# Performance work log

Hardware: AMD Instinct MI355X
Metric: run time of the kernel (lower is better)

The kernel has to match this reference:

```python
import jax, jax.numpy as jnp
import numpy as np

NUM_KNOTS = 256
DEGREE = 3
NUM_BASIS = NUM_KNOTS - DEGREE - 1  # 252
N = 1_048_576


def setup_inputs() -> dict:
    key = jax.random.key(0)
    # evaluation points in [-pi, pi), shape [N, 1] like the torch module
    x = jax.random.uniform(key, (N, 1), jnp.float32, -np.pi, np.pi)
    # knot vector: constant buffer from __init__
    knots = jnp.linspace(-np.pi, np.pi, NUM_KNOTS, dtype=jnp.float32)
    return {"x": x, "knots": knots}


def reference(x, knots):
    """Cox-de Boor B-spline basis, computed bottom-up (dynamic programming).

    Mathematically identical to the naive recursion in the torch module:
    same indicator base case ([knots[j], knots[j+1])) and same denominator>0
    guards, but each level is computed once and fully vectorized over N and j.
    """
    xs = x[:, 0]  # [N]
    # degree-0 basis: indicator of half-open knot interval -> [N, K-1]
    B = ((knots[:-1] <= xs[:, None]) & (xs[:, None] < knots[1:])).astype(jnp.float32)
    for k in range(1, DEGREE + 1):
        m = NUM_KNOTS - 1 - k  # number of basis functions at level k
        d1 = knots[k:k + m] - knots[:m]          # knots[j+k]   - knots[j]
        d2 = knots[k + 1:k + 1 + m] - knots[1:1 + m]  # knots[j+k+1] - knots[j+1]
        w1 = jnp.where(d1 > 0, (xs[:, None] - knots[:m]) / jnp.where(d1 > 0, d1, 1.0), 0.0)
        w2 = jnp.where(d2 > 0, (knots[k + 1:k + 1 + m] - xs[:, None]) / jnp.where(d2 > 0, d2, 1.0), 0.0)
        B = w1 * B[:, :m] + w2 * B[:, 1:1 + m]
    # level DEGREE already has exactly NUM_BASIS columns
    return B[:, :NUM_BASIS]
```

## Files before the change

kernel.cpp:

```cpp
#include <hip/hip_runtime.h>


constexpr int NUM_KNOTS = 256;
constexpr int NUM_BASIS = 252;
constexpr int CHUNKS    = 63;
constexpr int ROWS      = 256;

typedef float f4 __attribute__((ext_vector_type(4)));

__global__ __launch_bounds__(256) void bspline_kernel(
    const float* __restrict__ X, const float* __restrict__ knots,
    float* __restrict__ out, int n)
{
    __shared__ float s_knots[NUM_KNOTS];
    __shared__ f4   s_vlo[ROWS];
    __shared__ f4   s_vhi[ROWS];
    __shared__ int2 s_cc[ROWS];

    const int tid  = threadIdx.x;
    const int base = blockIdx.x * ROWS;
    const int row  = base + tid;

    s_knots[tid] = knots[tid];
    __syncthreads();

    {
        float x    = X[min(row, n - 1)];
        float k0   = s_knots[0];
        float kend = s_knots[NUM_KNOTS - 1];
        float inv_h = (float)(NUM_KNOTS - 1) / (kend - k0);

        int j0 = (int)floorf((x - k0) * inv_h);
        j0 = min(max(j0, 0), NUM_KNOTS - 2);
        while (j0 > 0 && x < s_knots[j0]) --j0;
        while (j0 < NUM_KNOTS - 2 && x >= s_knots[j0 + 1]) ++j0;

        float cb[4] = {1.0f, 0.0f, 0.0f, 0.0f};
        #pragma unroll
        for (int k = 1; k <= 3; ++k) {
            #pragma unroll
            for (int i = 3; i >= 0; --i) {
                if (i > k) continue;
                int j = j0 - k + i;
                float plo = (i >= 1)     ? cb[i - 1] : 0.0f;
                float phi = (i <= k - 1) ? cb[i]     : 0.0f;
                float val = 0.0f;
                if (j >= 0 && j <= NUM_KNOTS - 2 - k) {
                    float kj  = s_knots[j];
                    float kj1 = s_knots[j + 1];
                    float kjk = s_knots[j + k];
                    float kk1 = s_knots[j + k + 1];
                    val = (x - kj) / (kjk - kj) * plo
                        + (kk1 - x) / (kk1 - kj1) * phi;
                }
                cb[i] = val;
            }
        }

        int s = j0 - 3;
        int a = s & 3;
        int clo = s >> 2;
        float lo0=cb[0], lo1=cb[1], lo2=cb[2], lo3=cb[3];
        float hi0=0.f, hi1=0.f, hi2=0.f, hi3=0.f;
        if (a & 2) { hi3=hi1; hi2=hi0; hi1=lo3; hi0=lo2;
                     lo3=lo1; lo2=lo0; lo1=0.f; lo0=0.f; }
        if (a & 1) { hi3=hi2; hi2=hi1; hi1=hi0; hi0=lo3;
                     lo3=lo2; lo2=lo1; lo1=lo0; lo0=0.f; }
        f4 vlo; vlo.x=lo0; vlo.y=lo1; vlo.z=lo2; vlo.w=lo3;
        f4 vhi; vhi.x=hi0; vhi.y=hi1; vhi.z=hi2; vhi.w=hi3;
        s_vlo[tid] = vlo;
        s_vhi[tid] = vhi;
        s_cc[tid]  = make_int2(clo, clo + 1);
    }
    __syncthreads();

    int r = tid / CHUNKS;
    int c = tid - r * CHUNKS;
    f4* dst = (f4*)(out + (size_t)base * NUM_BASIS) + tid;
    const bool full = (base + ROWS <= n);

    #pragma unroll 3
    for (int it = 0; it < CHUNKS; ++it) {
        f4   vlo = s_vlo[r];
        f4   vhi = s_vhi[r];
        int2 cc  = s_cc[r];
        bool blo = (c == cc.x);
        bool bhi = (c == cc.y);
        f4 v;
        #pragma unroll
        for (int t = 0; t < 4; ++t)
            v[t] = blo ? vlo[t] : (bhi ? vhi[t] : 0.0f);
        if (full || base + r < n)
            dst[0] = v;
        dst += 256;
        r += 4; c += 4;
        if (c >= CHUNKS) { c -= CHUNKS; ++r; }
    }
}

extern "C" void kernel_launch(void* const* d_in, const int* in_sizes, int n_in,
                              void* d_out, int out_size, void* d_ws, size_t ws_size,
                              hipStream_t stream) {
    const float* x     = (const float*)d_in[0];
    const float* knots = (const float*)d_in[1];
    float* out = (float*)d_out;
    int n = in_sizes[0];
    int grid = (n + ROWS - 1) / ROWS;
    bspline_kernel<<<grid, 256, 0, stream>>>(x, knots, out, n);
}
```

Measured before the change: 202.8 us.

## Zero-fill output tile with wide stores then scatter nonzero basis chunks

Replaces the per-element select-based tile write with two phases. First, each block zero-fills its whole output tile using contiguous 64-byte-per-thread stores. Then, after a block barrier, each thread writes only its row's two nonzero float4 chunks directly to global memory. This removes the LDS staging and per-element selects, at the cost of writing those chunks twice and relying on the barrier to order the two global writes.

```diff
diff --git a/kernel.cpp b/kernel.cpp
--- a/kernel.cpp
+++ b/kernel.cpp
@@ -5,6 +5,7 @@
 constexpr int NUM_BASIS = 252;
 constexpr int CHUNKS    = 63;
 constexpr int ROWS      = 256;
+constexpr int TILE_F4   = ROWS * CHUNKS;
 
 typedef float f4 __attribute__((ext_vector_type(4)));
 
@@ -13,9 +14,6 @@
     float* __restrict__ out, int n)
 {
     __shared__ float s_knots[NUM_KNOTS];
-    __shared__ f4   s_vlo[ROWS];
-    __shared__ f4   s_vhi[ROWS];
-    __shared__ int2 s_cc[ROWS];
 
     const int tid  = threadIdx.x;
     const int base = blockIdx.x * ROWS;
@@ -24,77 +22,74 @@
     s_knots[tid] = knots[tid];
     __syncthreads();
 
-    {
-        float x    = X[min(row, n - 1)];
-        float k0   = s_knots[0];
-        float kend = s_knots[NUM_KNOTS - 1];
-        float inv_h = (float)(NUM_KNOTS - 1) / (kend - k0);
+    float x    = X[min(row, n - 1)];
+    float k0   = s_knots[0];
+    float kend = s_knots[NUM_KNOTS - 1];
+    float inv_h = (float)(NUM_KNOTS - 1) / (kend - k0);
 
-        int j0 = (int)floorf((x - k0) * inv_h);
-        j0 = min(max(j0, 0), NUM_KNOTS - 2);
-        while (j0 > 0 && x < s_knots[j0]) --j0;
-        while (j0 < NUM_KNOTS - 2 && x >= s_knots[j0 + 1]) ++j0;
+    int j0 = (int)floorf((x - k0) * inv_h);
+    j0 = min(max(j0, 0), NUM_KNOTS - 2);
+    while (j0 > 0 && x < s_knots[j0]) --j0;
+    while (j0 < NUM_KNOTS - 2 && x >= s_knots[j0 + 1]) ++j0;
 
-        float cb[4] = {1.0f, 0.0f, 0.0f, 0.0f};
+    float cb[4] = {1.0f, 0.0f, 0.0f, 0.0f};
+    #pragma unroll
+    for (int k = 1; k <= 3; ++k) {
         #pragma unroll
-        for (int k = 1; k <= 3; ++k) {
-            #pragma unroll
-            for (int i = 3; i >= 0; --i) {
-                if (i > k) continue;
-                int j = j0 - k + i;
-                float plo = (i >= 1)     ? cb[i - 1] : 0.0f;
-                float phi = (i <= k - 1) ? cb[i]     : 0.0f;
-                float val = 0.0f;
-                if (j >= 0 && j <= NUM_KNOTS - 2 - k) {
-                    float kj  = s_knots[j];
-                    float kj1 = s_knots[j + 1];
-                    float kjk = s_knots[j + k];
-                    float kk1 = s_knots[j + k + 1];
-                    val = (x - kj) / (kjk - kj) * plo
-                        + (kk1 - x) / (kk1 - kj1) * phi;
-                }
-                cb[i] = val;
+        for (int i = 3; i >= 0; --i) {
+            if (i > k) continue;
+            int j = j0 - k + i;
+            float plo = (i >= 1)     ? cb[i - 1] : 0.0f;
+            float phi = (i <= k - 1) ? cb[i]     : 0.0f;
+            float val = 0.0f;
+            if (j >= 0 && j <= NUM_KNOTS - 2 - k) {
+                float kj  = s_knots[j];
+                float kj1 = s_knots[j + 1];
+                float kjk = s_knots[j + k];
+                float kk1 = s_knots[j + k + 1];
+                val = (x - kj) / (kjk - kj) * plo
+                    + (kk1 - x) / (kk1 - kj1) * phi;
             }
+            cb[i] = val;
         }
+    }
 
-        int s = j0 - 3;
-        int a = s & 3;
-        int clo = s >> 2;
-        float lo0=cb[0], lo1=cb[1], lo2=cb[2], lo3=cb[3];
-        float hi0=0.f, hi1=0.f, hi2=0.f, hi3=0.f;
-        if (a & 2) { hi3=hi1; hi2=hi0; hi1=lo3; hi0=lo2;
-                     lo3=lo1; lo2=lo0; lo1=0.f; lo0=0.f; }
-        if (a & 1) { hi3=hi2; hi2=hi1; hi1=hi0; hi0=lo3;
-                     lo3=lo2; lo2=lo1; lo1=lo0; lo0=0.f; }
-        f4 vlo; vlo.x=lo0; vlo.y=lo1; vlo.z=lo2; vlo.w=lo3;
-        f4 vhi; vhi.x=hi0; vhi.y=hi1; vhi.z=hi2; vhi.w=hi3;
-        s_vlo[tid] = vlo;
-        s_vhi[tid] = vhi;
-        s_cc[tid]  = make_int2(clo, clo + 1);
+    int s = j0 - 3;
+    int a = s & 3;
+    int clo = s >> 2;
+    float lo0=cb[0], lo1=cb[1], lo2=cb[2], lo3=cb[3];
+    float hi0=0.f, hi1=0.f, hi2=0.f, hi3=0.f;
+    if (a & 2) { hi3=hi1; hi2=hi0; hi1=lo3; hi0=lo2;
+                 lo3=lo1; lo2=lo0; lo1=0.f; lo0=0.f; }
+    if (a & 1) { hi3=hi2; hi2=hi1; hi1=hi0; hi0=lo3;
+                 lo3=lo2; lo2=lo1; lo1=lo0; lo0=0.f; }
+    f4 vlo; vlo.x=lo0; vlo.y=lo1; vlo.z=lo2; vlo.w=lo3;
+    f4 vhi; vhi.x=hi0; vhi.y=hi1; vhi.z=hi2; vhi.w=hi3;
+
+    f4 z = (f4)0.0f;
+    f4* tile = (f4*)(out + (size_t)base * NUM_BASIS);
+    const bool full = (base + ROWS <= n);
+    if (full) {
+        f4* dst = tile + tid * 4;
+        #pragma unroll
+        for (int it = 0; it < 15; ++it) {
+            dst[0] = z; dst[1] = z; dst[2] = z; dst[3] = z;
+            dst += 1024;
+        }
+        if (tid < (TILE_F4 - 15 * 1024) / 4) {
+            f4* d2 = tile + 15 * 1024 + tid * 4;
+            d2[0] = z; d2[1] = z; d2[2] = z; d2[3] = z;
+        }
+    } else {
+        int lim = (n - base) * CHUNKS;
+        for (int i = tid; i < lim; i += 256) tile[i] = z;
     }
     __syncthreads();
 
-    int r = tid / CHUNKS;
-    int c = tid - r * CHUNKS;
-    f4* dst = (f4*)(out + (size_t)base * NUM_BASIS) + tid;
-    const bool full = (base + ROWS <= n);
-
-    #pragma unroll 3
-    for (int it = 0; it < CHUNKS; ++it) {
-        f4   vlo = s_vlo[r];
-        f4   vhi = s_vhi[r];
-        int2 cc  = s_cc[r];
-        bool blo = (c == cc.x);
-        bool bhi = (c == cc.y);
-        f4 v;
-        #pragma unroll
-        for (int t = 0; t < 4; ++t)
-            v[t] = blo ? vlo[t] : (bhi ? vhi[t] : 0.0f);
-        if (full || base + r < n)
-            dst[0] = v;
-        dst += 256;
-        r += 4; c += 4;
-        if (c >= CHUNKS) { c -= CHUNKS; ++r; }
+    if (row < n) {
+        f4* rowp = (f4*)(out + (size_t)row * NUM_BASIS);
+        if (clo >= 0)         rowp[clo]     = vlo;
+        if (clo < CHUNKS - 1) rowp[clo + 1] = vhi;
     }
 }
 
```

New measurement: 312.8 us. 1.54x slower.
